# Kernel optimization log

Hardware: AMD Instinct MI355X
Metric: run time of the kernel (lower is better)

Reference implementation:

```python
import jax, jax.numpy as jnp
import numpy as np

B, C, T = 1024, 64, 275
S = 10            # number of subjects
EMB = 184         # encoder embedding dim
PROJ = 1024       # projector dim
LN_EPS = 1e-5


def setup_inputs() -> dict:
    key = jax.random.key(0)
    ks = jax.random.split(key, 12)
    sc = lambda *shape: 1.0 / np.sqrt(shape[-1] if len(shape) > 1 else 1.0)
    return {
        "eeg": jax.random.normal(ks[0], (B, C, T), dtype=jnp.float32),
        "subject_ids": jax.random.randint(ks[1], (B,), 0, S, dtype=jnp.int64),
        # per-subject Linear(T, T): y = x @ W.T + b
        "subj_W": jax.random.normal(ks[2], (S, T, T), dtype=jnp.float32) / np.sqrt(T),
        "subj_b": jax.random.normal(ks[3], (S, T), dtype=jnp.float32) * 0.02,
        # encoder stub: flatten (C*T) -> Linear -> EMB
        "enc_W": jax.random.normal(ks[4], (C * T, EMB), dtype=jnp.float32) / np.sqrt(C * T),
        "enc_b": jnp.zeros((EMB,), dtype=jnp.float32),
        # projector: Linear(EMB, PROJ) -> ResidualAdd(GELU -> Linear(PROJ, PROJ)) -> LayerNorm
        "W1": jax.random.normal(ks[5], (EMB, PROJ), dtype=jnp.float32) / np.sqrt(EMB),
        "b1": jnp.zeros((PROJ,), dtype=jnp.float32),
        "W2": jax.random.normal(ks[6], (PROJ, PROJ), dtype=jnp.float32) / np.sqrt(PROJ),
        "b2": jnp.zeros((PROJ,), dtype=jnp.float32),
        "gamma": jnp.ones((PROJ,), dtype=jnp.float32),
        "beta": jnp.zeros((PROJ,), dtype=jnp.float32),
    }


def reference(eeg, subject_ids, subj_W, subj_b, enc_W, enc_b, W1, b1, W2, b2, gamma, beta):
    # --- subject-wise alignment: grouped gather -> linear -> scatter ---
    # Vectorized form of the per-subject loop: each row b uses weight subj_W[sid[b]].
    Wg = subj_W[subject_ids]              # [B, T, T]
    bg = subj_b[subject_ids]              # [B, T]
    # torch Linear: y = x @ W.T + b  ->  y[b,c,u] = sum_t eeg[b,c,t] * Wg[b,u,t]
    x = jnp.einsum("bct,but->bcu", eeg, Wg) + bg[:, None, :]   # [B, C, T]

    # --- encoder stub (SpatioTemporalCNN placeholder): flatten + linear ---
    h = x.reshape(x.shape[0], -1) @ enc_W + enc_b              # [B, EMB]

    # --- MLPProjector ---
    h = h @ W1 + b1                                            # [B, PROJ]
    r = jax.nn.gelu(h, approximate=False) @ W2 + b2            # dropout is identity at eval
    h = h + r
    # LayerNorm over last dim
    mu = jnp.mean(h, axis=-1, keepdims=True)
    var = jnp.mean(jnp.square(h - mu), axis=-1, keepdims=True)
    out = (h - mu) * jax.lax.rsqrt(var + LN_EPS) * gamma + beta
    return out
```

## Files before the change

### kernel.cpp

```cpp
#include <hip/hip_runtime.h>
#include <math.h>

#define B_N    1024
#define C_N    64
#define T_N    275
#define S_N    10
#define EMB_N  184
#define PROJ_N 1024
#define CT_N   (C_N * T_N)
#define TP     288
#define KP2    (C_N * TP)
#define EMBP   192
#define KZ2    16
#define KC2    (KP2 / KZ2)
#define KZ5    2
#define GMAX   264

#define SEC_W   0
#define SEC_E   810
#define SEC_1   1002
#define SEC_2   1050
#define SEC_G   1306
#define SEC_N   1307

typedef unsigned short u16;
typedef __attribute__((ext_vector_type(8))) short short8;
typedef __attribute__((ext_vector_type(4))) short short4v;
typedef __attribute__((ext_vector_type(4))) float f32x4;

#define MFMA16(a,b,c) __builtin_amdgcn_mfma_f32_16x16x32_bf16(a, b, c, 0, 0, 0)

__device__ __forceinline__ u16 f2bf(float f) {
    union { float f; unsigned u; } v; v.f = f;
    unsigned r = v.u + 0x7FFFu + ((v.u >> 16) & 1u);
    return (u16)(r >> 16);
}
__device__ __forceinline__ float gelu_exact(float v) {
    return 0.5f * v * (1.0f + erff(v * 0.70710678118654752f));
}
__device__ __forceinline__ void gload16(const void* g, void* lds) {
    __builtin_amdgcn_global_load_lds(
        (const __attribute__((address_space(1))) void*)g,
        (__attribute__((address_space(3))) void*)lds, 16, 0, 0);
}
__device__ __forceinline__ short8 cv8(const float* v) {
    short8 r;
    #pragma unroll
    for (int e = 0; e < 8; ++e) r[e] = (short)f2bf(v[e]);
    return r;
}

__global__ __launch_bounds__(256) void p_all(
    const int* __restrict__ sid, const float* __restrict__ W,
    const float* __restrict__ encW, const float* __restrict__ W1,
    const float* __restrict__ W2, const float* __restrict__ subj_b,
    u16* __restrict__ Wb, u16* __restrict__ eT, u16* __restrict__ w1t,
    u16* __restrict__ w2t, int* __restrict__ bsq, float* __restrict__ sbp)
{
    __shared__ char smem[16640];
    const int blk = blockIdx.x;
    const int tid = threadIdx.x;

    if (blk < SEC_E) {
        int idx4 = blk * 256 + tid;
        if (idx4 >= S_N * TP * TP / 4) return;
        int o = idx4 * 4;
        int row = o / TP, t = o - row * TP;
        int s = row / TP, u = row - s * TP;
        short4v pk;
        #pragma unroll
        for (int e = 0; e < 4; ++e) {
            float v = (u < T_N && t + e < T_N)
                ? W[((size_t)s * T_N + u) * T_N + t + e] : 0.f;
            pk[e] = (short)f2bf(v);
        }
        *reinterpret_cast<short4v*>(Wb + o) = pk;
        return;
    }
    if (blk < SEC_1) {
        float (*tile)[65] = (float(*)[65])smem;
        int local = blk - SEC_E;
        const int c = local / 3;
        const int n0 = (local % 3) * 64;
        for (int u0 = 0; u0 < TP; u0 += 64) {
            int wlen = (TP - u0 < 64) ? (TP - u0) : 64;
            __syncthreads();
            for (int l = tid; l < 4096; l += 256) {
                int i = l >> 6, j = l & 63;
                int u = u0 + i, n = n0 + j;
                float v = 0.f;
                if (u < T_N && n < EMB_N)
                    v = encW[((size_t)c * T_N + u) * EMB_N + n];
                tile[i][j] = v;
            }
            __syncthreads();
            for (int l = tid; l < 4096; l += 256) {
                int j = l >> 6, i = l & 63;
                if (i < wlen)
                    eT[(size_t)(n0 + j) * KP2 + (size_t)c * TP + u0 + i] =
                        f2bf(tile[i][j]);
            }
        }
        return;
    }
    if (blk < SEC_2) {
        float (*tile)[65] = (float(*)[65])smem;
        int local = blk - SEC_1;
        const int k0 = (local % 3) * 64, n0 = (local / 3) * 64;
        for (int l = tid; l < 4096; l += 256) {
            int i = l >> 6, j = l & 63;
            float v = (k0 + i < EMB_N) ? W1[(size_t)(k0 + i) * PROJ_N + n0 + j] : 0.f;
            tile[i][j] = v;
        }
        __syncthreads();
        for (int l = tid; l < 4096; l += 256) {
            int j = l >> 6, i = l & 63;
            w1t[(size_t)(n0 + j) * EMBP + k0 + i] = f2bf(tile[i][j]);
        }
        return;
    }
    if (blk < SEC_G) {
        float (*tile)[65] = (float(*)[65])smem;
        int local = blk - SEC_2;
        const int k0 = (local % 16) * 64, n0 = (local / 16) * 64;
        for (int l = tid; l < 4096; l += 256) {
            int i = l >> 6, j = l & 63;
            tile[i][j] = W2[(size_t)(k0 + i) * PROJ_N + n0 + j];
        }
        __syncthreads();
        for (int l = tid; l < 4096; l += 256) {
            int j = l >> 6, i = l & 63;
            w2t[(size_t)(n0 + j) * PROJ_N + k0 + i] = f2bf(tile[i][j]);
        }
        return;
    }
    {
        for (int i = tid; i < S_N * TP; i += 256) {
            int s = i / TP, u = i - s * TP;
            sbp[i] = (u < T_N) ? subj_b[s * T_N + u] : 0.f;
        }
        int* sgrp = (int*)smem;
        int* C    = (int*)(smem + 4096);
        int* tot  = (int*)(smem + 4096 + 640);
        for (int i = tid; i < 1024; i += 256) sgrp[i] = sid[i];
        for (int i = tid; i < 4 * GMAX; i += 256) bsq[i] = -1;
        __syncthreads();
        const int w4 = tid >> 6, lane = tid & 63;
        #pragma unroll
        for (int j = 0; j < 4; ++j) {
            int chunk = w4 * 4 + j;
            int sb = sgrp[chunk * 64 + lane];
            int myc = 0;
            for (int s = 0; s < S_N; ++s) {
                unsigned long long m = __ballot(sb == s);
                if (lane == s) myc = (int)__popcll(m);
            }
            if (lane < S_N) C[chunk * S_N + lane] = myc;
        }
        __syncthreads();
        if (tid < S_N) {
            int a = 0;
            for (int w2 = 0; w2 < 16; ++w2) a += C[w2 * S_N + tid];
            tot[tid] = a;
        }
        __syncthreads();
        #pragma unroll
        for (int rep = 0; rep < 4; ++rep) {
            int b = tid + rep * 256;
            int s = sgrp[b];
            int off = 0;
            for (int s2 = 0; s2 < S_N; ++s2)
                if (s2 < s) off += (tot[s2] + 3) & ~3;
            int chunk = b >> 6;
            int rank = 0;
            for (int w2 = 0; w2 < 16; ++w2)
                if (w2 < chunk) rank += C[w2 * S_N + s];
            for (int i = chunk * 64; i < b; ++i) rank += (sgrp[i] == s) ? 1 : 0;
            bsq[off + rank] = b;
        }
    }
}

__global__ __launch_bounds__(256, 3) void k1d(
    const float* __restrict__ eeg, const int* __restrict__ sid,
    const u16* __restrict__ Wb, const float* __restrict__ sbp,
    const int* __restrict__ bsq, u16* __restrict__ xb)
{
    const int g = blockIdx.x;
    const int b0 = bsq[g * 4];
    if (b0 < 0) return;
    const int p = blockIdx.y >> 1, ch = blockIdx.y & 1;
    const int s = sid[b0];
    const int tid = threadIdx.x;
    const int w = tid >> 6, lane = tid & 63;
    const int bi = w >> 1, uh = w & 1;
    const int lrow = lane & 15, lk = lane >> 4;
    const int b = bsq[g * 4 + p * 2 + bi];
    const int bs = (b >= 0) ? b : b0;

    const float* e0 = eeg + (size_t)bs * CT_N + (ch * 32 + lrow) * T_N;
    const float* e1 = e0 + 16 * T_N;
    const u16* Wr = Wb + (size_t)s * TP * TP + (size_t)(uh * 144 + lrow) * TP;

    #define K1_ELOAD(ks)                                                       \
        {   const int tbase = (ks) * 32 + lk * 8;                              \
            if ((ks) < 8) {                                                    \
                _Pragma("unroll")                                              \
                for (int e = 0; e < 8; ++e) {                                  \
                    ea[e] = e0[tbase + e];                                     \
                    eb[e] = e1[tbase + e];                                     \
                }                                                              \
            } else {                                                           \
                _Pragma("unroll")                                              \
                for (int e = 0; e < 8; ++e) {                                  \
                    int t_ = tbase + e;                                        \
                    ea[e] = (t_ < T_N) ? e0[t_] : 0.f;                         \
                    eb[e] = (t_ < T_N) ? e1[t_] : 0.f;                         \
                }                                                              \
            }                                                                  \
        }
    #define K1_WLOAD(ks)                                                       \
        _Pragma("unroll")                                                      \
        for (int uf = 0; uf < 9; ++uf)                                         \
            wv[uf] = *reinterpret_cast<const short8*>(                         \
                Wr + (size_t)uf * 16 * TP + (ks) * 32 + lk * 8);

    f32x4 acc[9][2] = {};
    float ea[8], eb[8];
    short8 wv[9];

    K1_ELOAD(0);
    K1_WLOAD(0);

    #pragma unroll
    for (int ks = 0; ks < 9; ++ks) {
        short8 ef0 = cv8(ea), ef1 = cv8(eb);
        if (ks < 8) K1_ELOAD(ks + 1);
        #pragma unroll
        for (int uf = 0; uf < 9; ++uf) {
            acc[uf][0] = MFMA16(wv[uf], ef0, acc[uf][0]);
            acc[uf][1] = MFMA16(wv[uf], ef1, acc[uf][1]);
        }
        if (ks < 8) K1_WLOAD(ks + 1);
    }

    if (b < 0) return;
    u16* xrow = xb + (size_t)b * KP2 + (size_t)(ch * 32) * TP;
    #pragma unroll
    for (int uf = 0; uf < 9; ++uf) {
        int ub = uh * 144 + uf * 16 + 4 * lk;
        float4 b4 = *reinterpret_cast<const float4*>(sbp + s * TP + ub);
        float bias[4] = { b4.x, b4.y, b4.z, b4.w };
        #pragma unroll
        for (int cf = 0; cf < 2; ++cf) {
            int c = cf * 16 + lrow;
            short4v pk;
            #pragma unroll
            for (int r = 0; r < 4; ++r)
                pk[r] = (ub + r < T_N) ? (short)f2bf(acc[uf][cf][r] + bias[r])
                                       : (short)0;
            *reinterpret_cast<short4v*>(xrow + (size_t)c * TP + ub) = pk;
        }
    }
    #undef K1_ELOAD
    #undef K1_WLOAD
}

__global__ __launch_bounds__(256) void k2_mfma(
    const u16* __restrict__ xb, const u16* __restrict__ eT,
    float* __restrict__ part)
{
    __shared__ __align__(16) u16 Ab[2][64 * 64];
    const int m0 = blockIdx.x * 64;
    const int kz = blockIdx.y;
    const int kbase = kz * KC2;
    const int tid = threadIdx.x;
    const int w = tid >> 6, lane = tid & 63;
    const int lrow = lane & 15, lk = lane >> 4;

    #define K2_STAGE(st, step)                                                 \
        _Pragma("unroll")                                                      \
        for (int p = 0; p < 2; ++p) {                                          \
            int l = tid + p * 256;                                             \
            int r_ = l >> 3, q_ = l & 7;                                       \
            gload16(xb + (size_t)(m0 + r_) * KP2 + kbase + (step) * 64 +       \
                        ((q_ ^ (r_ & 7)) << 3),                                \
                    &Ab[st][l * 8]);                                           \
        }
    #define K2_BLOAD(step, dst)                                                \
        _Pragma("unroll")                                                      \
        for (int ct = 0; ct < 3; ++ct)                                         \
            _Pragma("unroll")                                                  \
            for (int ki = 0; ki < 2; ++ki)                                     \
                dst[ct][ki] = *reinterpret_cast<const short8*>(                \
                    eT + (size_t)(48 * w + 16 * ct + lrow) * KP2 + kbase +     \
                    (step) * 64 + ki * 32 + 8 * lk);

    f32x4 acc[4][3] = {};
    short8 bf[3][2], bn[3][2];

    K2_STAGE(0, 0);
    K2_BLOAD(0, bf);
    __syncthreads();

    for (int step = 0; step < 18; ++step) {
        const int st = step & 1;
        if (step < 17) {
            K2_STAGE(st ^ 1, step + 1);
            K2_BLOAD(step + 1, bn);
        }
        #pragma unroll
        for (int ki = 0; ki < 2; ++ki)
            #pragma unroll
            for (int rt = 0; rt < 4; ++rt) {
                int m = 16 * rt + lrow;
                int chunk = m * 8 + ((4 * ki + lk) ^ (m & 7));
                short8 af = *reinterpret_cast<const short8*>(&Ab[st][chunk * 8]);
                #pragma unroll
                for (int ct = 0; ct < 3; ++ct)
                    acc[rt][ct] = MFMA16(af, bf[ct][ki], acc[rt][ct]);
            }
        __syncthreads();
        #pragma unroll
        for (int ct = 0; ct < 3; ++ct)
            #pragma unroll
            for (int ki = 0; ki < 2; ++ki) bf[ct][ki] = bn[ct][ki];
    }

    #pragma unroll
    for (int rt = 0; rt < 4; ++rt)
        #pragma unroll
        for (int ct = 0; ct < 3; ++ct) {
            int n = 48 * w + 16 * ct + lrow;
            #pragma unroll
            for (int r = 0; r < 4; ++r) {
                int m = m0 + 16 * rt + 4 * lk + r;
                part[((size_t)kz * B_N + m) * EMBP + n] = acc[rt][ct][r];
            }
        }
    #undef K2_STAGE
    #undef K2_BLOAD
}

__global__ __launch_bounds__(256) void k3_reduce(
    const float* __restrict__ part, const float* __restrict__ enc_b,
    u16* __restrict__ hb)
{
    int idx = blockIdx.x * 256 + threadIdx.x;
    if (idx >= B_N * EMBP) return;
    int n = idx % EMBP;
    float s = 0.f;
    if (n < EMB_N) {
        s = enc_b[n];
        #pragma unroll
        for (int z = 0; z < KZ2; ++z)
            s += part[(size_t)z * B_N * EMBP + idx];
    }
    hb[idx] = f2bf(s);
}

__global__ __launch_bounds__(256) void k4_mfma(
    const u16* __restrict__ hb, const u16* __restrict__ w1t,
    const float* __restrict__ b1, float* __restrict__ h1, u16* __restrict__ g)
{
    __shared__ __align__(16) u16 Ab[64 * EMBP];
    __shared__ __align__(16) u16 Bb[64 * EMBP];
    const int m0 = blockIdx.x * 64, n0 = blockIdx.y * 64;
    const int tid = threadIdx.x;
    const int w = tid >> 6, lane = tid & 63;
    const int wr = w >> 1, wc = w & 1;
    const int lrow = lane & 15, lk = lane >> 4;

    #pragma unroll
    for (int i = 0; i < 6; ++i) {
        int L = tid + i * 256;
        int row = L / 24, qp = L % 24;
        int ql = qp ^ (row & 7);
        gload16(hb  + (size_t)(m0 + row) * EMBP + ql * 8, &Ab[(size_t)L * 8]);
        gload16(w1t + (size_t)(n0 + row) * EMBP + ql * 8, &Bb[(size_t)L * 8]);
    }
    __syncthreads();

    f32x4 acc[2][2] = {};
    #pragma unroll
    for (int ks = 0; ks < 6; ++ks) {
        #pragma unroll
        for (int rt = 0; rt < 2; ++rt) {
            int c = 32 * wr + 16 * rt + lrow;
            short8 af = *reinterpret_cast<const short8*>(
                &Ab[c * EMBP + (((4 * ks + lk) ^ (c & 7)) * 8)]);
            #pragma unroll
            for (int ct = 0; ct < 2; ++ct) {
                int nl = 32 * wc + 16 * ct + lrow;
                short8 bfv = *reinterpret_cast<const short8*>(
                    &Bb[nl * EMBP + (((4 * ks + lk) ^ (nl & 7)) * 8)]);
                acc[rt][ct] = MFMA16(af, bfv, acc[rt][ct]);
            }
        }
    }
    #pragma unroll
    for (int rt = 0; rt < 2; ++rt)
        #pragma unroll
        for (int ct = 0; ct < 2; ++ct) {
            int n = n0 + 32 * wc + 16 * ct + lrow;
            #pragma unroll
            for (int r = 0; r < 4; ++r) {
                int m = m0 + 32 * wr + 16 * rt + 4 * lk + r;
                float v = acc[rt][ct][r] + b1[n];
                size_t o = (size_t)m * PROJ_N + n;
                h1[o] = v;
                g[o] = f2bf(gelu_exact(v));
            }
        }
}

__global__ __launch_bounds__(256) void k5_mfma(
    const u16* __restrict__ g, const u16* __restrict__ w2t,
    float* __restrict__ part2)
{
    __shared__ __align__(16) u16 Ab[2][64 * 64];
    __shared__ __align__(16) u16 Bb[2][64 * 64];
    const int m0 = blockIdx.x * 64, n0 = blockIdx.y * 64;
    const int kz = blockIdx.z;
    const int kbase = kz * (PROJ_N / KZ5);
    const int tid = threadIdx.x;
    const int w = tid >> 6, lane = tid & 63;
    const int wr = w >> 1, wc = w & 1;
    const int lrow = lane & 15, lk = lane >> 4;

    const int r0 = tid >> 3, q0 = tid & 7;
    const int r1 = (tid + 256) >> 3;
    const u16* a0 = g + (size_t)(m0 + r0) * PROJ_N + (q0 ^ (r0 & 7)) * 8;
    const u16* a1 = g + (size_t)(m0 + r1) * PROJ_N + (q0 ^ (r1 & 7)) * 8;
    const u16* b0 = w2t + (size_t)(n0 + r0) * PROJ_N + (q0 ^ (r0 & 7)) * 8;
    const u16* b1p = w2t + (size_t)(n0 + r1) * PROJ_N + (q0 ^ (r1 & 7)) * 8;

    f32x4 acc[2][2] = {};
    int buf = 0;
    gload16(a0 + kbase, &Ab[0][(size_t)(w * 64) * 8]);
    gload16(a1 + kbase, &Ab[0][(size_t)(w * 64 + 256) * 8]);
    gload16(b0 + kbase, &Bb[0][(size_t)(w * 64) * 8]);
    gload16(b1p + kbase, &Bb[0][(size_t)(w * 64 + 256) * 8]);
    __syncthreads();

    for (int step = 0; step < 8; ++step) {
        if (step < 7) {
            int k0 = kbase + (step + 1) * 64;
            gload16(a0 + k0, &Ab[buf ^ 1][(size_t)(w * 64) * 8]);
            gload16(a1 + k0, &Ab[buf ^ 1][(size_t)(w * 64 + 256) * 8]);
            gload16(b0 + k0, &Bb[buf ^ 1][(size_t)(w * 64) * 8]);
            gload16(b1p + k0, &Bb[buf ^ 1][(size_t)(w * 64 + 256) * 8]);
        }
        #pragma unroll
        for (int ki = 0; ki < 2; ++ki) {
            #pragma unroll
            for (int rt = 0; rt < 2; ++rt) {
                int c = 32 * wr + 16 * rt + lrow;
                short8 af = *reinterpret_cast<const short8*>(
                    &Ab[buf][c * 64 + (((lk + 4 * ki) ^ (c & 7)) * 8)]);
                #pragma unroll
                for (int ct = 0; ct < 2; ++ct) {
                    int nl = 32 * wc + 16 * ct + lrow;
                    short8 bfv = *reinterpret_cast<const short8*>(
                        &Bb[buf][nl * 64 + (((lk + 4 * ki) ^ (nl & 7)) * 8)]);
                    acc[rt][ct] = MFMA16(af, bfv, acc[rt][ct]);
                }
            }
        }
        __syncthreads();
        buf ^= 1;
    }
    #pragma unroll
    for (int rt = 0; rt < 2; ++rt)
        #pragma unroll
        for (int ct = 0; ct < 2; ++ct) {
            int n = n0 + 32 * wc + 16 * ct + lrow;
            #pragma unroll
            for (int r = 0; r < 4; ++r) {
                int m = m0 + 32 * wr + 16 * rt + 4 * lk + r;
                part2[(size_t)kz * B_N * PROJ_N + (size_t)m * PROJ_N + n] = acc[rt][ct][r];
            }
        }
}

__global__ __launch_bounds__(256) void k5r_ln(
    const float* __restrict__ part2, const float* __restrict__ h1,
    const float* __restrict__ b2, const float* __restrict__ gamma,
    const float* __restrict__ beta, float* __restrict__ out)
{
    const int m = blockIdx.x;
    const int tid = threadIdx.x;
    const float4* h4 = reinterpret_cast<const float4*>(h1 + (size_t)m * PROJ_N);
    const float4* p0 = reinterpret_cast<const float4*>(part2 + (size_t)m * PROJ_N);
    const float4* p1 = reinterpret_cast<const float4*>(part2 + (size_t)(B_N + m) * PROJ_N);
    const float4* b4 = reinterpret_cast<const float4*>(b2);
    float4 va = h4[tid], vb = p0[tid], vc = p1[tid], vd = b4[tid];
    float v[4] = { va.x + vb.x + vc.x + vd.x, va.y + vb.y + vc.y + vd.y,
                   va.z + vb.z + vc.z + vd.z, va.w + vb.w + vc.w + vd.w };
    float s = 0.f, sq = 0.f;
    #pragma unroll
    for (int i = 0; i < 4; ++i) { s += v[i]; sq += v[i] * v[i]; }
    #pragma unroll
    for (int off = 32; off > 0; off >>= 1) {
        s  += __shfl_down(s, off);
        sq += __shfl_down(sq, off);
    }
    __shared__ float ss[4], ssq[4];
    int wid = tid >> 6, lane = tid & 63;
    if (lane == 0) { ss[wid] = s; ssq[wid] = sq; }
    __syncthreads();
    if (tid == 0) {
        float a = 0.f, bsum = 0.f;
        #pragma unroll
        for (int q = 0; q < 4; ++q) { a += ss[q]; bsum += ssq[q]; }
        ss[0] = a; ssq[0] = bsum;
    }
    __syncthreads();
    float mu  = ss[0] * (1.0f / PROJ_N);
    float var = ssq[0] * (1.0f / PROJ_N) - mu * mu;
    float rs  = rsqrtf(var + 1e-5f);
    const float4 g4 = reinterpret_cast<const float4*>(gamma)[tid];
    const float4 be4 = reinterpret_cast<const float4*>(beta)[tid];
    float gg[4] = { g4.x, g4.y, g4.z, g4.w };
    float bb[4] = { be4.x, be4.y, be4.z, be4.w };
    float4 o4;
    float* op = reinterpret_cast<float*>(&o4);
    #pragma unroll
    for (int i = 0; i < 4; ++i) op[i] = (v[i] - mu) * rs * gg[i] + bb[i];
    reinterpret_cast<float4*>(out + (size_t)m * PROJ_N)[tid] = o4;
}

extern "C" void kernel_launch(void* const* d_in, const int* in_sizes, int n_in,
                              void* d_out, int out_size, void* d_ws, size_t ws_size,
                              hipStream_t stream)
{
    const float* eeg    = (const float*)d_in[0];
    const int*   sid    = (const int*)  d_in[1];
    const float* subj_W = (const float*)d_in[2];
    const float* subj_b = (const float*)d_in[3];
    const float* enc_W  = (const float*)d_in[4];
    const float* enc_b  = (const float*)d_in[5];
    const float* W1     = (const float*)d_in[6];
    const float* b1     = (const float*)d_in[7];
    const float* W2     = (const float*)d_in[8];
    const float* b2     = (const float*)d_in[9];
    const float* gamma  = (const float*)d_in[10];
    const float* beta   = (const float*)d_in[11];
    float* out = (float*)d_out;

    char* w = (char*)d_ws;
    u16*   xb    = (u16*)(w);
    u16*   Wb    = (u16*)(w + 37748736);
    u16*   eT    = (u16*)(w + 39407616);
    u16*   w1t   = (u16*)(w + 46485504);
    u16*   w2t   = (u16*)(w + 46878720);
    u16*   hb    = (u16*)(w + 48975872);
    float* h1    = (float*)(w + 49369088);
    u16*   g     = (u16*)(w + 53563392);
    float* sbp   = (float*)(w + 55660544);
    int*   bsq   = (int*)(w + 55672064);
    float* part  = (float*)(w + 55676288);
    float* part2 = (float*)(w + 68259200);

    p_all<<<dim3(SEC_N), 256, 0, stream>>>(sid, subj_W, enc_W, W1, W2, subj_b,
                                           Wb, eT, w1t, w2t, bsq, sbp);
    k1d  <<<dim3(GMAX, 4), 256, 0, stream>>>(eeg, sid, Wb, sbp, bsq, xb);
    k2_mfma<<<dim3(16, KZ2), 256, 0, stream>>>(xb, eT, part);
    k3_reduce<<<dim3((B_N * EMBP + 255) / 256), 256, 0, stream>>>(part, enc_b, hb);
    k4_mfma<<<dim3(16, 16), 256, 0, stream>>>(hb, w1t, b1, h1, g);
    k5_mfma<<<dim3(16, 16, KZ5), 256, 0, stream>>>(g, w2t, part2);
    k5r_ln <<<dim3(B_N), 256, 0, stream>>>(part2, h1, b2, gamma, beta, out);
}
```

Baseline: 135.7 us.

## Replace subject-grouped alignment kernel with per-sample grid mapped across XCDs

The subject-alignment GEMM kernel no longer uses the subject-sorted batch list. It now launches 3072 blocks, one per sample and 96-column output slice, with the block index swizzled so consecutive samples land on different XCDs. Each wave covers 48 output columns over 32 channels, so it keeps 3x2 accumulators instead of 9x2, and launch bounds rise to 4 blocks per CU. The explicit software prefetch of the next k-step is dropped, and per-subject weight reuse across grouped samples is lost, in exchange for more parallelism and higher occupancy.

```diff
diff --git a/kernel.cpp b/kernel.cpp
--- a/kernel.cpp
+++ b/kernel.cpp
@@ -181,79 +181,64 @@
     }
 }
 
-__global__ __launch_bounds__(256, 3) void k1d(
+__global__ __launch_bounds__(256, 4) void k1t(
     const float* __restrict__ eeg, const int* __restrict__ sid,
     const u16* __restrict__ Wb, const float* __restrict__ sbp,
-    const int* __restrict__ bsq, u16* __restrict__ xb)
-{
-    const int g = blockIdx.x;
-    const int b0 = bsq[g * 4];
-    if (b0 < 0) return;
-    const int p = blockIdx.y >> 1, ch = blockIdx.y & 1;
-    const int s = sid[b0];
+    u16* __restrict__ xb)
+{
+    const int blk = blockIdx.x;
+    const int xcd = blk & 7, ion = blk >> 3;
+    const int q = ion / 3, u96 = ion - 3 * q;
+    const int b = q * 8 + xcd;
+    const int s = sid[b];
     const int tid = threadIdx.x;
     const int w = tid >> 6, lane = tid & 63;
-    const int bi = w >> 1, uh = w & 1;
+    const int ch = w >> 1, uq = w & 1;
+    const int u0 = u96 * 96 + uq * 48;
     const int lrow = lane & 15, lk = lane >> 4;
-    const int b = bsq[g * 4 + p * 2 + bi];
-    const int bs = (b >= 0) ? b : b0;
-
-    const float* e0 = eeg + (size_t)bs * CT_N + (ch * 32 + lrow) * T_N;
+
+    const float* e0 = eeg + (size_t)b * CT_N + (ch * 32 + lrow) * T_N;
     const float* e1 = e0 + 16 * T_N;
-    const u16* Wr = Wb + (size_t)s * TP * TP + (size_t)(uh * 144 + lrow) * TP;
-
-    #define K1_ELOAD(ks)                                                       \
-        {   const int tbase = (ks) * 32 + lk * 8;                              \
-            if ((ks) < 8) {                                                    \
-                _Pragma("unroll")                                              \
-                for (int e = 0; e < 8; ++e) {                                  \
-                    ea[e] = e0[tbase + e];                                     \
-                    eb[e] = e1[tbase + e];                                     \
-                }                                                              \
-            } else {                                                           \
-                _Pragma("unroll")                                              \
-                for (int e = 0; e < 8; ++e) {                                  \
-                    int t_ = tbase + e;                                        \
-                    ea[e] = (t_ < T_N) ? e0[t_] : 0.f;                         \
-                    eb[e] = (t_ < T_N) ? e1[t_] : 0.f;                         \
-                }                                                              \
-            }                                                                  \
-        }
-    #define K1_WLOAD(ks)                                                       \
-        _Pragma("unroll")                                                      \
-        for (int uf = 0; uf < 9; ++uf)                                         \
-            wv[uf] = *reinterpret_cast<const short8*>(                         \
-                Wr + (size_t)uf * 16 * TP + (ks) * 32 + lk * 8);
-
-    f32x4 acc[9][2] = {};
+    const u16* Wr = Wb + (size_t)s * TP * TP + (size_t)(u0 + lrow) * TP;
+
+    f32x4 acc[3][2] = {};
     float ea[8], eb[8];
-    short8 wv[9];
-
-    K1_ELOAD(0);
-    K1_WLOAD(0);
+    short8 wv[3];
 
     #pragma unroll
     for (int ks = 0; ks < 9; ++ks) {
+        const int tb = ks * 32 + lk * 8;
+        if (ks < 8) {
+            #pragma unroll
+            for (int e = 0; e < 8; ++e) { ea[e] = e0[tb + e]; eb[e] = e1[tb + e]; }
+        } else {
+            #pragma unroll
+            for (int e = 0; e < 8; ++e) {
+                ea[e] = (tb + e < T_N) ? e0[tb + e] : 0.f;
+                eb[e] = (tb + e < T_N) ? e1[tb + e] : 0.f;
+            }
+        }
+        #pragma unroll
+        for (int uf = 0; uf < 3; ++uf)
+            wv[uf] = *reinterpret_cast<const short8*>(
+                Wr + (size_t)uf * 16 * TP + ks * 32 + lk * 8);
         short8 ef0 = cv8(ea), ef1 = cv8(eb);
-        if (ks < 8) K1_ELOAD(ks + 1);
-        #pragma unroll
-        for (int uf = 0; uf < 9; ++uf) {
+        #pragma unroll
+        for (int uf = 0; uf < 3; ++uf) {
             acc[uf][0] = MFMA16(wv[uf], ef0, acc[uf][0]);
             acc[uf][1] = MFMA16(wv[uf], ef1, acc[uf][1]);
         }
-        if (ks < 8) K1_WLOAD(ks + 1);
-    }
-
-    if (b < 0) return;
-    u16* xrow = xb + (size_t)b * KP2 + (size_t)(ch * 32) * TP;
-    #pragma unroll
-    for (int uf = 0; uf < 9; ++uf) {
-        int ub = uh * 144 + uf * 16 + 4 * lk;
+    }
+
+    u16* xrow = xb + (size_t)b * KP2;
+    #pragma unroll
+    for (int uf = 0; uf < 3; ++uf) {
+        int ub = u0 + uf * 16 + 4 * lk;
         float4 b4 = *reinterpret_cast<const float4*>(sbp + s * TP + ub);
         float bias[4] = { b4.x, b4.y, b4.z, b4.w };
         #pragma unroll
         for (int cf = 0; cf < 2; ++cf) {
-            int c = cf * 16 + lrow;
+            int c = ch * 32 + cf * 16 + lrow;
             short4v pk;
             #pragma unroll
             for (int r = 0; r < 4; ++r)
@@ -262,8 +247,6 @@
             *reinterpret_cast<short4v*>(xrow + (size_t)c * TP + ub) = pk;
         }
     }
-    #undef K1_ELOAD
-    #undef K1_WLOAD
 }
 
 __global__ __launch_bounds__(256) void k2_mfma(
@@ -564,7 +547,7 @@
 
     p_all<<<dim3(SEC_N), 256, 0, stream>>>(sid, subj_W, enc_W, W1, W2, subj_b,
                                            Wb, eT, w1t, w2t, bsq, sbp);
-    k1d  <<<dim3(GMAX, 4), 256, 0, stream>>>(eeg, sid, Wb, sbp, bsq, xb);
+    k1t  <<<dim3(3072), 256, 0, stream>>>(eeg, sid, Wb, sbp, xb);
     k2_mfma<<<dim3(16, KZ2), 256, 0, stream>>>(xb, eT, part);
     k3_reduce<<<dim3((B_N * EMBP + 255) / 256), 256, 0, stream>>>(part, enc_b, hb);
     k4_mfma<<<dim3(16, 16), 256, 0, stream>>>(hb, w1t, b1, h1, g);
```

Measured after the change: 155.1 us. +14.3%, slower.
